# Optimization experiments

Hardware: AMD Instinct MI355X
Metric: run time of the kernel (lower is better)

Reference implementation:

```python
import jax, jax.numpy as jnp
import numpy as np

BATCH, SEQ, DIM = 2, 2048, 1024
HEADS, HEAD_DIM = 16, 64
K_NEI = 64
SCALE = 1.0 / float(np.sqrt(HEAD_DIM))


def _cantor_routes(seq_len: int, k: int, depth: int = 8) -> np.ndarray:
    """Replicates _build_positional_routes: Cantor coords + topk smallest |ci-cj|."""
    pos = np.arange(seq_len, dtype=np.float64)
    x = pos / max(1, seq_len - 1)
    x = np.clip(x, 1e-6, 1.0 - 1e-6)
    val = np.zeros_like(x)
    factor = 0.5
    for _ in range(depth):
        xs = x * 3.0
        digit = np.floor(xs)
        x = xs - digit
        val = val + (digit == 2.0).astype(np.float64) * factor
        factor *= 0.5
    val = np.clip(val, 0.0, 1.0)
    dist = np.abs(val[:, None] - val[None, :])  # [S, S]
    routes = np.argsort(dist, axis=1, kind='stable')[:, :k]  # smallest-k neighbors
    return routes.astype(np.int32)


def setup_inputs() -> dict:
    key = jax.random.key(0)
    kx, kw1, kb1, kw2, kb2 = jax.random.split(key, 5)
    x = jax.random.normal(kx, (BATCH, SEQ, DIM), dtype=jnp.float32)
    qkv_w = jax.random.normal(kw1, (3 * DIM, DIM), dtype=jnp.float32) * 0.02
    qkv_b = jax.random.normal(kb1, (3 * DIM,), dtype=jnp.float32) * 0.02
    out_w = jax.random.normal(kw2, (DIM, DIM), dtype=jnp.float32) * 0.02
    out_b = jax.random.normal(kb2, (DIM,), dtype=jnp.float32) * 0.02
    routes = jnp.asarray(_cantor_routes(SEQ, K_NEI))  # [S, K] int32
    return {"x": x, "routes": routes, "qkv_w": qkv_w, "qkv_b": qkv_b,
            "out_w": out_w, "out_b": out_b}


def reference(x, routes, qkv_w, qkv_b, out_w, out_b):
    B, S, _ = x.shape
    # QKV projection (torch Linear: x @ W.T + b)
    qkv = x @ qkv_w.T + qkv_b                          # [B, S, 3*DIM]
    qkv = qkv.reshape(B, S, 3, HEADS, HEAD_DIM).transpose(2, 0, 3, 1, 4)
    q, k, v = qkv[0], qkv[1], qkv[2]                   # each [B, H, S, D]
    # Gather K/V along precomputed Cantor routes: [B, H, S, K, D]
    k_g = jnp.take(k, routes, axis=2)
    v_g = jnp.take(v, routes, axis=2)
    scores = jnp.einsum('bhqd,bhqkd->bhqk', q, k_g) * SCALE
    attn = jax.nn.softmax(scores, axis=-1)             # [B, H, S, K]
    out = jnp.einsum('bhqk,bhqkd->bhqd', attn, v_g)    # [B, H, S, D]
    out = out.transpose(0, 2, 1, 3).reshape(B, S, DIM)
    return out @ out_w.T + out_b
```

## Files before the change

### kernel.cpp

```cpp
#include <hip/hip_runtime.h>
#include <math.h>

#define BATCH    2
#define SEQ      2048
#define DIM      1024
#define HEADS    16
#define HEAD_DIM 64
#define K_NEI    64
#define QKV_DIM  3072
#define MROWS    (BATCH * SEQ)
#define ATT_SCALE 0.125f
#define CHUNK    16
#define MAXCH    2048

typedef _Float16 half8  __attribute__((ext_vector_type(8)));
typedef _Float16 half4  __attribute__((ext_vector_type(4)));
typedef float    floatx4 __attribute__((ext_vector_type(4)));

__device__ inline void async_copy16(const void* g, void* l) {
  __builtin_amdgcn_global_load_lds(
      (const __attribute__((address_space(1))) unsigned int*)g,
      (__attribute__((address_space(3))) unsigned int*)l, 16, 0, 0);
}

__global__ __launch_bounds__(256)
void cast3_group(const float* __restrict__ a, int na4,
                 const float* __restrict__ b, int nb4,
                 const float* __restrict__ c, int nc4,
                 _Float16* __restrict__ oa, _Float16* __restrict__ ob,
                 _Float16* __restrict__ oc,
                 const int* __restrict__ routes, int* __restrict__ gq) {
  if (blockIdx.x < 8) {
    const int q = blockIdx.x * 256 + threadIdx.x;
    const int lead = routes[q * K_NEI];
    bool same = (lead >= 0) && (lead < SEQ);
    if (same && lead != q) {
      const int4* pa = (const int4*)(routes + q * K_NEI);
      const int4* pb = (const int4*)(routes + lead * K_NEI);
#pragma unroll
      for (int t = 0; t < 16; t++) {
        int4 x = pa[t], y = pb[t];
        same = same && (x.x == y.x) && (x.y == y.y) && (x.z == y.z) && (x.w == y.w);
      }
    }
    gq[q] = same ? lead : q;
  }

  const int total = na4 + nb4 + nc4;
  for (int i = blockIdx.x * blockDim.x + threadIdx.x; i < total;
       i += gridDim.x * blockDim.x) {
    const float* src; _Float16* dst; int idx;
    if (i < na4)            { src = a; dst = oa; idx = i; }
    else if (i < na4 + nb4) { src = b; dst = ob; idx = i - na4; }
    else                    { src = c; dst = oc; idx = i - na4 - nb4; }
    float4 v = *(const float4*)(src + (size_t)idx * 4);
    half4 o;
    o[0] = (_Float16)v.x; o[1] = (_Float16)v.y;
    o[2] = (_Float16)v.z; o[3] = (_Float16)v.w;
    *(half4*)(dst + (size_t)idx * 4) = o;
  }
}

template<int BM, int BN, bool HALF_OUT>
__global__ __launch_bounds__(256)
void gemm_bt_f16(const _Float16* __restrict__ A, const _Float16* __restrict__ B,
                 const float* __restrict__ bias, void* __restrict__ Cv,
                 int M, int N, int K) {
  constexpr int FI = BM / 32;
  constexpr int FJ = BN / 32;
  constexpr int CA = BM / 64;
  constexpr int CB = BN / 64;
  __shared__ _Float16 As[2 * BM * 32];
  __shared__ _Float16 Bs[2 * BN * 32];

  const int tid  = threadIdx.x;
  const int lane = tid & 63;
  const int w    = tid >> 6;
  const int wr   = w >> 1;
  const int wc   = w & 1;
  const int bm   = blockIdx.y * BM;
  const int bn   = blockIdx.x * BN;

  const int srow = w * 16 + (lane >> 2);
  const int scol = (lane & 3) * 8;
  const _Float16* ga = A + (size_t)(bm + srow) * K + scol;
  const _Float16* gb = B + (size_t)(bn + srow) * K + scol;

  const int frow = lane & 15;
  const int fk   = (lane >> 4) * 8;

  floatx4 acc[FI][FJ] = {};

  for (int k0 = 0; k0 < K; k0 += 64) {
#pragma unroll
    for (int sub = 0; sub < 2; sub++) {
      const int kk = k0 + sub * 32;
#pragma unroll
      for (int i = 0; i < CA; i++)
        async_copy16(ga + (size_t)(i * 64) * K + kk,
                     As + sub * BM * 32 + w * 512 + i * 2048);
#pragma unroll
      for (int i = 0; i < CB; i++)
        async_copy16(gb + (size_t)(i * 64) * K + kk,
                     Bs + sub * BN * 32 + w * 512 + i * 2048);
    }
    __syncthreads();

#pragma unroll
    for (int sub = 0; sub < 2; sub++) {
      half8 af[FI], bf[FJ];
#pragma unroll
      for (int i = 0; i < FI; i++)
        af[i] = *(const half8*)&As[sub * BM * 32 + (wr * (BM / 2) + i * 16 + frow) * 32 + fk];
#pragma unroll
      for (int j = 0; j < FJ; j++)
        bf[j] = *(const half8*)&Bs[sub * BN * 32 + (wc * (BN / 2) + j * 16 + frow) * 32 + fk];
#pragma unroll
      for (int i = 0; i < FI; i++)
#pragma unroll
        for (int j = 0; j < FJ; j++) {
          if (HALF_OUT)
            acc[i][j] = __builtin_amdgcn_mfma_f32_16x16x32_f16(bf[j], af[i], acc[i][j], 0, 0, 0);
          else
            acc[i][j] = __builtin_amdgcn_mfma_f32_16x16x32_f16(af[i], bf[j], acc[i][j], 0, 0, 0);
        }
    }
    __syncthreads();
  }

  if (HALF_OUT) {
    _Float16* C = (_Float16*)Cv;
    const int mloc = lane & 15;
    const int nloc = (lane >> 4) * 4;
#pragma unroll
    for (int j = 0; j < FJ; j++) {
      const int gcol = bn + wc * (BN / 2) + j * 16 + nloc;
      float4 bj = *(const float4*)(bias + gcol);
#pragma unroll
      for (int i = 0; i < FI; i++) {
        const int grow = bm + wr * (BM / 2) + i * 16 + mloc;
        half4 hv;
        hv[0] = (_Float16)(acc[i][j][0] + bj.x);
        hv[1] = (_Float16)(acc[i][j][1] + bj.y);
        hv[2] = (_Float16)(acc[i][j][2] + bj.z);
        hv[3] = (_Float16)(acc[i][j][3] + bj.w);
        *(half4*)(C + (size_t)grow * N + gcol) = hv;
      }
    }
  } else {
    float* C = (float*)Cv;
    const int crow = (lane >> 4) * 4;
    const int ccol = lane & 15;
#pragma unroll
    for (int j = 0; j < FJ; j++) {
      const int gcol = bn + wc * (BN / 2) + j * 16 + ccol;
      const float bj = bias[gcol];
#pragma unroll
      for (int i = 0; i < FI; i++) {
        const int grow = bm + wr * (BM / 2) + i * 16 + crow;
        float* cp = C + (size_t)grow * N + gcol;
#pragma unroll
        for (int r = 0; r < 4; r++)
          cp[(size_t)r * N] = acc[i][j][r] + bj;
      }
    }
  }
}

__global__ __launch_bounds__(256)
void group_emit(const int* __restrict__ gq, int* __restrict__ gmem,
                int* __restrict__ chunks, int* __restrict__ meta) {
  __shared__ int cnt[SEQ];
  __shared__ int base[SEQ];
  __shared__ int warpsum[8];
  __shared__ int nch_sm;
  const int tid = threadIdx.x;

  for (int i = tid; i < SEQ; i += 256) cnt[i] = 0;
  if (tid == 0) nch_sm = 0;
  __syncthreads();

  for (int q = tid; q < SEQ; q += 256) atomicAdd(&cnt[gq[q]], 1);
  __syncthreads();

  int local[8];
  int s = 0;
#pragma unroll
  for (int k = 0; k < 8; k++) { local[k] = s; s += cnt[tid * 8 + k]; }
  const int lane = tid & 63, wv = tid >> 6;
  int sc = s;
#pragma unroll
  for (int off = 1; off < 64; off <<= 1) {
    int t2 = __shfl_up(sc, off);
    if (lane >= off) sc += t2;
  }
  if (lane == 63) warpsum[wv] = sc;
  __syncthreads();
  int wvoff = 0;
  for (int k = 0; k < wv; k++) wvoff += warpsum[k];
  const int thrbase = wvoff + sc - s;
#pragma unroll
  for (int k = 0; k < 8; k++) base[tid * 8 + k] = thrbase + local[k];
  __syncthreads();

  for (int gg = tid; gg < SEQ; gg += 256) {
    const int c = cnt[gg];
    if (c > 0) {
      const int nchk = (c + CHUNK - 1) / CHUNK;
      const int slot = atomicAdd(&nch_sm, nchk);
      for (int k2 = 0; k2 < nchk; k2++) {
        const int sidx = slot + k2;
        if (sidx < MAXCH) {
          const int len = min(CHUNK, c - k2 * CHUNK);
          chunks[2 * sidx]     = gg;
          chunks[2 * sidx + 1] = (base[gg] + k2 * CHUNK) | (len << 16);
        }
      }
    }
  }
  __syncthreads();
  if (tid == 0) meta[0] = min(nch_sm, MAXCH);

  for (int q = tid; q < SEQ; q += 256) {
    const int slot = atomicAdd(&base[gq[q]], 1);
    gmem[slot] = q;
  }
}

__global__ __launch_bounds__(128)
void attn_mfma(const _Float16* __restrict__ qkv, const int* __restrict__ routes,
               const int* __restrict__ gmem, const int* __restrict__ chunks,
               const int* __restrict__ meta, _Float16* __restrict__ ao) {
  __shared__ _Float16 lds[2][9216];

  const int tid  = threadIdx.x;
  const int w    = tid >> 6;
  const int lane = tid & 63;
  const int g    = lane >> 4;
  const int c    = lane & 15;

  _Float16* Ks = &lds[w][0];
  _Float16* Vs = &lds[w][4096];
  _Float16* Ps = &lds[w][8192];

  const int nch    = meta[0];
  const int njobs  = nch * 32;
  const int nwaves = gridDim.x * 2;

  const int c8   = (lane & 7) ^ ((lane >> 3) & 7);
  const int rsub = lane >> 3;

  for (int job = blockIdx.x * 2 + w; job < njobs; job += nwaves) {
    const int ch = job >> 5;
    const int bh = job & 31;
    const int h  = bh & 15;
    const int b  = bh >> 4;

    const int gid   = chunks[2 * ch];
    const int mpack = chunks[2 * ch + 1];
    const int mbase = mpack & 0xFFFF;
    const int mlen  = mpack >> 16;
    const size_t rowb = (size_t)b * SEQ;

    const int rt_l = routes[gid * K_NEI + lane];
    const int qm_l = gmem[mbase + min(c, mlen - 1)];

#pragma unroll
    for (int k = 0; k < 8; k++) {
      const int row = __shfl(rt_l, 8 * k + rsub);
      const _Float16* kp = qkv + (rowb + row) * QKV_DIM + DIM + h * HEAD_DIM + c8 * 8;
      async_copy16(kp,       Ks + k * 512);
      async_copy16(kp + DIM, Vs + k * 512);
    }

    const _Float16* qrow = qkv + (rowb + qm_l) * QKV_DIM + h * HEAD_DIM + g * 8;
    const half8 qf0 = *(const half8*)(qrow);
    const half8 qf1 = *(const half8*)(qrow + 32);

    asm volatile("s_waitcnt vmcnt(0)" ::: "memory");

    floatx4 st[4] = {};
    const half8 qf[2] = { qf0, qf1 };
    __builtin_amdgcn_s_setprio(1);
#pragma unroll
    for (int s2 = 0; s2 < 2; s2++) {
#pragma unroll
      for (int m = 0; m < 4; m++) {
        const int r = m * 16 + c;
        const half8 kf =
            *(const half8*)&Ks[r * 64 + ((((s2 << 2) + g) ^ (c & 7)) << 3)];
        st[m] = __builtin_amdgcn_mfma_f32_16x16x32_f16(kf, qf[s2], st[m], 0, 0, 0);
      }
    }
    __builtin_amdgcn_s_setprio(0);

    float mx = st[0][0];
#pragma unroll
    for (int m = 0; m < 4; m++)
#pragma unroll
      for (int r = 0; r < 4; r++) mx = fmaxf(mx, st[m][r]);
    mx = fmaxf(mx, __shfl_xor(mx, 16));
    mx = fmaxf(mx, __shfl_xor(mx, 32));

    float p[16];
    float sum = 0.f;
#pragma unroll
    for (int m = 0; m < 4; m++)
#pragma unroll
      for (int r = 0; r < 4; r++) {
        const float e = __expf((st[m][r] - mx) * ATT_SCALE);
        p[m * 4 + r] = e;
        sum += e;
      }
    sum += __shfl_xor(sum, 16);
    sum += __shfl_xor(sum, 32);
    const float inv = 1.0f / sum;

#pragma unroll
    for (int m = 0; m < 4; m++) {
      half4 ph;
      ph[0] = (_Float16)(p[m * 4 + 0] * inv);
      ph[1] = (_Float16)(p[m * 4 + 1] * inv);
      ph[2] = (_Float16)(p[m * 4 + 2] * inv);
      ph[3] = (_Float16)(p[m * 4 + 3] * inv);
      const int idx = c * 64 + (((2 * m + (g >> 1)) ^ (c & 7)) << 3) + ((g & 1) << 2);
      *(half4*)&Ps[idx] = ph;
    }
    asm volatile("s_waitcnt lgkmcnt(0)" ::: "memory");

    half8 pf[2];
#pragma unroll
    for (int s2 = 0; s2 < 2; s2++)
      pf[s2] = *(const half8*)&Ps[c * 64 + ((((s2 << 2) + g) ^ (c & 7)) << 3)];

    floatx4 oa[4] = {};
    __builtin_amdgcn_s_setprio(1);
#pragma unroll
    for (int n = 0; n < 4; n++) {
      const int dtop = 2 * n + (c >> 3);
#pragma unroll
      for (int s2 = 0; s2 < 2; s2++) {
        half8 vf;
#pragma unroll
        for (int j = 0; j < 8; j++) {
          const int rr = s2 * 32 + g * 8 + j;
          vf[j] = Vs[rr * 64 + ((dtop ^ j) << 3) + (c & 7)];
        }
        oa[n] = __builtin_amdgcn_mfma_f32_16x16x32_f16(pf[s2], vf, oa[n], 0, 0, 0);
      }
    }
    __builtin_amdgcn_s_setprio(0);

#pragma unroll
    for (int r = 0; r < 4; r++) {
      const int i = g * 4 + r;
      const int qrow_i = __shfl(qm_l, i);
      if (i < mlen) {
        _Float16* op = ao + (rowb + qrow_i) * DIM + h * HEAD_DIM + c;
#pragma unroll
        for (int n = 0; n < 4; n++) op[n * 16] = (_Float16)oa[n][r];
      }
    }
  }
}

extern "C" void kernel_launch(void* const* d_in, const int* in_sizes, int n_in,
                              void* d_out, int out_size, void* d_ws, size_t ws_size,
                              hipStream_t stream) {
  const float* x      = (const float*)d_in[0];
  const int*   routes = (const int*)  d_in[1];
  const float* qkv_w  = (const float*)d_in[2];
  const float* qkv_b  = (const float*)d_in[3];
  const float* out_w  = (const float*)d_in[4];
  const float* out_b  = (const float*)d_in[5];
  float* out = (float*)d_out;

  _Float16* qkvh = (_Float16*)d_ws;
  _Float16* aoh  = qkvh + (size_t)MROWS * QKV_DIM;
  _Float16* xh   = aoh  + (size_t)MROWS * DIM;
  _Float16* wh   = xh   + (size_t)MROWS * DIM;
  _Float16* owh  = wh   + (size_t)QKV_DIM * DIM;

  char* scr   = (char*)d_out + (size_t)out_size - 65536;
  int* gq     = (int*)scr;
  int* gmem   = gq + SEQ;
  int* chunks = gmem + SEQ;
  int* meta   = chunks + 2 * MAXCH;

  cast3_group<<<1024, 256, 0, stream>>>(x, MROWS * DIM / 4,
                                        qkv_w, QKV_DIM * DIM / 4,
                                        out_w, DIM * DIM / 4,
                                        xh, wh, owh, routes, gq);

  group_emit<<<1, 256, 0, stream>>>(gq, gmem, chunks, meta);

  {
    dim3 g(QKV_DIM / 128, MROWS / 128);
    gemm_bt_f16<128, 128, true><<<g, 256, 0, stream>>>(xh, wh, qkv_b, qkvh,
                                                       MROWS, QKV_DIM, DIM);
  }

  attn_mfma<<<4096, 128, 0, stream>>>(qkvh, routes, gmem, chunks, meta, aoh);

  {
    dim3 g(DIM / 128, MROWS / 64);
    gemm_bt_f16<64, 128, false><<<g, 256, 0, stream>>>(aoh, owh, out_b, out,
                                                       MROWS, DIM, DIM);
  }
}
```

Measured before the change: 177.2 us.

## Replace QKV GEMM with 256x256-tile double-buffered 512-thread MFMA kernel

Adds a dedicated QKV projection GEMM that uses 256x256 output tiles and 8 waves per block. K-tiles are double-buffered in LDS through async global-to-LDS copies, split K halves are interleaved with the barrier, and s_setprio raises priority around the MFMA bursts. The epilogue adds bias and writes fp16 outputs with vectorized half4 stores. The larger tile improves data reuse per byte loaded. In exchange it uses 128KB of LDS per block and launches only 192 blocks, which may leave some CUs idle and limit occupancy.

Result: slower. 188.5 us (+6.4%).

```diff
diff --git a/kernel.cpp b/kernel.cpp
--- a/kernel.cpp
+++ b/kernel.cpp
@@ -167,6 +167,118 @@
   }
 }
 
+__global__ __launch_bounds__(512, 2)
+void gemm_qkv_dp(const _Float16* __restrict__ A, const _Float16* __restrict__ B,
+                 const float* __restrict__ bias, _Float16* __restrict__ C,
+                 int M, int N, int K) {
+  __shared__ _Float16 As[2][256 * 64];
+  __shared__ _Float16 Bs[2][256 * 64];
+
+  const int tid  = threadIdx.x;
+  const int lane = tid & 63;
+  const int w    = tid >> 6;
+  const int wr   = w >> 2;
+  const int wc   = w & 3;
+  const int bm   = blockIdx.y * 256;
+  const int bn   = blockIdx.x * 256;
+
+  const int srow = tid >> 3;
+  const int scs  = tid & 7;
+  const _Float16* ga = A + (size_t)(bm + srow) * K + scs * 8;
+  const _Float16* gb = B + (size_t)(bn + srow) * K + scs * 8;
+
+  const int frow  = lane & 15;
+  const int fk    = (lane >> 4) * 8;
+  const int abase = (wr * 128 + frow) * 64 + fk;
+  const int bbase = (wc * 64  + frow) * 64 + fk;
+
+  const int NT = K / 64;
+
+  auto qstage = [&](int buf, int kt) {
+    const int kofs = kt * 64;
+    _Float16* da = &As[buf][tid * 8];
+    _Float16* db = &Bs[buf][tid * 8];
+#pragma unroll
+    for (int i = 0; i < 4; i++) {
+      async_copy16(ga + (size_t)(i * 64) * K + kofs, da + i * 4096);
+      async_copy16(gb + (size_t)(i * 64) * K + kofs, db + i * 4096);
+    }
+  };
+
+  qstage(0, 0);
+  qstage(1, 1);
+  asm volatile("s_waitcnt vmcnt(8)" ::: "memory");
+  __builtin_amdgcn_s_barrier();
+  __builtin_amdgcn_sched_barrier(0);
+
+  floatx4 acc[8][4] = {};
+  int cur = 0;
+
+  for (int j = 0; j < NT; j++) {
+    const _Float16* as = As[cur];
+    const _Float16* bs = Bs[cur];
+    half8 af[8], bf[4];
+
+#pragma unroll
+    for (int mi = 0; mi < 8; mi++) af[mi] = *(const half8*)&as[abase + mi * 1024];
+#pragma unroll
+    for (int ni = 0; ni < 4; ni++) bf[ni] = *(const half8*)&bs[bbase + ni * 1024];
+    __builtin_amdgcn_s_setprio(1);
+#pragma unroll
+    for (int mi = 0; mi < 8; mi++)
+#pragma unroll
+      for (int ni = 0; ni < 4; ni++)
+        acc[mi][ni] = __builtin_amdgcn_mfma_f32_16x16x32_f16(bf[ni], af[mi], acc[mi][ni], 0, 0, 0);
+    __builtin_amdgcn_s_setprio(0);
+
+#pragma unroll
+    for (int mi = 0; mi < 8; mi++) af[mi] = *(const half8*)&as[abase + mi * 1024 + 32];
+#pragma unroll
+    for (int ni = 0; ni < 4; ni++) bf[ni] = *(const half8*)&bs[bbase + ni * 1024 + 32];
+
+    asm volatile("s_waitcnt lgkmcnt(0)" ::: "memory");
+    __builtin_amdgcn_sched_barrier(0);
+    __builtin_amdgcn_s_barrier();
+    __builtin_amdgcn_sched_barrier(0);
+
+    if (j + 2 < NT) qstage(cur, j + 2);
+
+    __builtin_amdgcn_s_setprio(1);
+#pragma unroll
+    for (int mi = 0; mi < 8; mi++)
+#pragma unroll
+      for (int ni = 0; ni < 4; ni++)
+        acc[mi][ni] = __builtin_amdgcn_mfma_f32_16x16x32_f16(bf[ni], af[mi], acc[mi][ni], 0, 0, 0);
+    __builtin_amdgcn_s_setprio(0);
+
+    if (j + 1 < NT) {
+      if (j + 2 < NT) asm volatile("s_waitcnt vmcnt(8)" ::: "memory");
+      else            asm volatile("s_waitcnt vmcnt(0)" ::: "memory");
+      __builtin_amdgcn_s_barrier();
+      __builtin_amdgcn_sched_barrier(0);
+    }
+    cur ^= 1;
+  }
+
+  const int mloc = lane & 15;
+  const int nloc = (lane >> 4) * 4;
+#pragma unroll
+  for (int ni = 0; ni < 4; ni++) {
+    const int gcol = bn + wc * 64 + ni * 16 + nloc;
+    float4 bj = *(const float4*)(bias + gcol);
+#pragma unroll
+    for (int mi = 0; mi < 8; mi++) {
+      const int grow = bm + wr * 128 + mi * 16 + mloc;
+      half4 hv;
+      hv[0] = (_Float16)(acc[mi][ni][0] + bj.x);
+      hv[1] = (_Float16)(acc[mi][ni][1] + bj.y);
+      hv[2] = (_Float16)(acc[mi][ni][2] + bj.z);
+      hv[3] = (_Float16)(acc[mi][ni][3] + bj.w);
+      *(half4*)(C + (size_t)grow * N + gcol) = hv;
+    }
+  }
+}
+
 __global__ __launch_bounds__(256)
 void group_emit(const int* __restrict__ gq, int* __restrict__ gmem,
                 int* __restrict__ chunks, int* __restrict__ meta) {
@@ -395,9 +507,9 @@
   group_emit<<<1, 256, 0, stream>>>(gq, gmem, chunks, meta);
 
   {
-    dim3 g(QKV_DIM / 128, MROWS / 128);
-    gemm_bt_f16<128, 128, true><<<g, 256, 0, stream>>>(xh, wh, qkv_b, qkvh,
-                                                       MROWS, QKV_DIM, DIM);
+    dim3 g(QKV_DIM / 256, MROWS / 256);
+    gemm_qkv_dp<<<g, 512, 0, stream>>>(xh, wh, qkv_b, qkvh,
+                                       MROWS, QKV_DIM, DIM);
   }
 
   attn_mfma<<<4096, 128, 0, stream>>>(qkvh, routes, gmem, chunks, meta, aoh);
```
